# Kernel optimization log

Measured on AMD Instinct MI355X. Metric: run time of the kernel, lower is better.

Reference implementation:

```python
import jax, jax.numpy as jnp
import numpy as np

B, N, E, H, ID = 32, 256, 512, 8, 8
D = E // H  # head dim = 64


def setup_inputs() -> dict:
    key = jax.random.key(0)
    ks = jax.random.split(key, 6)
    s = lambda k, shape, fan_in: jax.random.normal(k, shape, jnp.float32) * (fan_in ** -0.5)
    return {
        "x": jax.random.normal(ks[0], (B, N, E), jnp.float32),
        "U": jax.random.normal(ks[1], (B, N, N, ID), jnp.float32),
        "w_qkv": s(ks[2], (3 * E, E), E),   # nn.MultiheadAttention in_proj_weight
        "b_qkv": jnp.zeros((3 * E,), jnp.float32),
        "w_out": s(ks[3], (E, E), E),       # out_proj.weight
        "b_out": jnp.zeros((E,), jnp.float32),
        "w_u": s(ks[4], (H, ID), ID),       # u_proj.weight
        "b_u": jnp.zeros((H,), jnp.float32),
    }


def reference(x, U, w_qkv, b_qkv, w_out, b_out, w_u, b_u):
    # fused QKV projection (torch MHA uses a single in_proj)
    qkv = x @ w_qkv.T + b_qkv                      # [B,N,3E]
    q, k, v = jnp.split(qkv, 3, axis=-1)
    split_heads = lambda t: t.reshape(B, N, H, D).transpose(0, 2, 1, 3)  # [B,H,N,D]
    q, k, v = split_heads(q), split_heads(k), split_heads(v)
    # interaction tensor -> one additive bias per head: [B,N,N,H] -> [B,H,N,N]
    bias = (U @ w_u.T + b_u).transpose(0, 3, 1, 2)
    logits = jnp.einsum('bhnd,bhmd->bhnm', q, k) * (D ** -0.5) + bias  # [B,H,N,N]
    attn = jax.nn.softmax(logits, axis=-1)
    o = jnp.einsum('bhnm,bhmd->bhnd', attn, v)     # [B,H,N,D]
    o = o.transpose(0, 2, 1, 3).reshape(B, N, E)
    return o @ w_out.T + b_out
```

## Files before the change

kernel.cpp:

```cpp
#include <hip/hip_runtime.h>
#include <stdint.h>

#define Bn 32
#define Nn 256
#define En 512
#define Hn 8
#define Dn 64

typedef __attribute__((ext_vector_type(8))) short bf16x8;
typedef __attribute__((ext_vector_type(4))) short bf16x4;
typedef __attribute__((ext_vector_type(4))) float f32x4;
typedef __attribute__((ext_vector_type(4))) _Float16 h4f;

__device__ __forceinline__ unsigned short f2bf(float f){
  union{float f; uint32_t i;} v; v.f = f;
  uint32_t i = v.i;
  return (unsigned short)((i + 0x7fffu + ((i>>16)&1u)) >> 16);
}

__device__ __forceinline__ void stage16(const unsigned short* g,
                                        unsigned short* lds_wave_base,
                                        unsigned short* lds_lane){
#if __has_builtin(__builtin_amdgcn_global_load_lds)
  __builtin_amdgcn_global_load_lds(
      (const __attribute__((address_space(1))) unsigned int*)g,
      (__attribute__((address_space(3))) unsigned int*)lds_wave_base, 16, 0, 0);
  (void)lds_lane;
#else
  *(bf16x8*)lds_lane = *(const bf16x8*)g;
  (void)lds_wave_base;
#endif
}

__global__ __launch_bounds__(256) void convert_x(
    const float* __restrict__ x, unsigned short* __restrict__ xb){
  size_t i = ((size_t)blockIdx.x * 256 + threadIdx.x) * 8;
  float4 a = *(const float4*)(x + i);
  float4 b = *(const float4*)(x + i + 4);
  bf16x8 p;
  p[0]=(short)f2bf(a.x); p[1]=(short)f2bf(a.y); p[2]=(short)f2bf(a.z); p[3]=(short)f2bf(a.w);
  p[4]=(short)f2bf(b.x); p[5]=(short)f2bf(b.y); p[6]=(short)f2bf(b.z); p[7]=(short)f2bf(b.w);
  *(bf16x8*)(xb + i) = p;
}

__global__ __launch_bounds__(256) void prep_kernel(
    const float* __restrict__ x, unsigned short* __restrict__ xb,
    const float* __restrict__ U, const float* __restrict__ w_u,
    const float* __restrict__ b_u, unsigned short* __restrict__ bias16,
    const float* __restrict__ wq, unsigned short* __restrict__ wqb,
    const float* __restrict__ wo, unsigned short* __restrict__ wob){
  __shared__ float s_wu[64];
  __shared__ float s_bu[8];
  const int bx = blockIdx.x;
  const int tid = threadIdx.x;
  if (bx < 2048 || bx >= 4096) {
    const float* src; unsigned short* dst; size_t i;
    if (bx < 2048)      { src = x;  dst = xb;  i = ((size_t)bx * 256 + tid) * 8; }
    else if (bx < 4480) { src = wq; dst = wqb; i = ((size_t)(bx-4096) * 256 + tid) * 8; }
    else                { src = wo; dst = wob; i = ((size_t)(bx-4480) * 256 + tid) * 8; }
    float4 a = *(const float4*)(src + i);
    float4 b = *(const float4*)(src + i + 4);
    bf16x8 p;
    p[0]=(short)f2bf(a.x); p[1]=(short)f2bf(a.y); p[2]=(short)f2bf(a.z); p[3]=(short)f2bf(a.w);
    p[4]=(short)f2bf(b.x); p[5]=(short)f2bf(b.y); p[6]=(short)f2bf(b.z); p[7]=(short)f2bf(b.w);
    *(bf16x8*)(dst + i) = p;
    return;
  }
  if (tid < 64) s_wu[tid] = w_u[tid];
  if (tid < 8)  s_bu[tid] = b_u[tid];
  __syncthreads();
  const int t  = (bx - 2048) * 256 + tid;
  const int m_ = t & 255;
  const int n4 = (t >> 8) & 63;
  const int bb = t >> 14;
  const float* up = U + ((size_t)(bb*Nn + n4*4)*Nn + m_) * 8;
  float u[4][8];
  #pragma unroll
  for (int r = 0; r < 4; ++r) {
    float4 a = *(const float4*)(up + (size_t)r * (Nn*8));
    float4 c = *(const float4*)(up + (size_t)r * (Nn*8) + 4);
    u[r][0]=a.x; u[r][1]=a.y; u[r][2]=a.z; u[r][3]=a.w;
    u[r][4]=c.x; u[r][5]=c.y; u[r][6]=c.z; u[r][7]=c.w;
  }
  const int    lane_in = ((n4 & 3) * 16 + (m_ & 15)) * 4;
  const size_t tbase   = ((size_t)(n4 >> 2) * 16 + (m_ >> 4)) * 256;
  #pragma unroll
  for (int h = 0; h < 8; ++h) {
    const float bu = s_bu[h];
    float acc[4];
    #pragma unroll
    for (int r = 0; r < 4; ++r) {
      float a = bu;
      #pragma unroll
      for (int id = 0; id < 8; ++id) a += u[r][id] * s_wu[h*8 + id];
      acc[r] = a;
    }
    h4f hv;
    hv[0]=(_Float16)acc[0]; hv[1]=(_Float16)acc[1];
    hv[2]=(_Float16)acc[2]; hv[3]=(_Float16)acc[3];
    *(h4f*)(bias16 + (size_t)(bb*Hn + h) * 65536 + tbase + lane_in) = hv;
  }
}

__global__ __launch_bounds__(256) void qkv_gemm4(
    const unsigned short* __restrict__ xb, const unsigned short* __restrict__ wqb,
    const float* __restrict__ bq,
    unsigned short* __restrict__ q_ws, unsigned short* __restrict__ k_ws,
    unsigned short* __restrict__ v_ws){
  __shared__ unsigned short smem[32768];
  const int tid = threadIdx.x;
  const int bx = blockIdx.x;
  const int by = blockIdx.y;
  const int row0 = by * 128, n0 = bx * 128;
  const int lane = tid & 63, wv = tid >> 6;
  const int wr = wv >> 1, wc = wv & 1;
  const int lm = lane & 15, quad = lane >> 4;
  f32x4 acc[4][4] = {};

  auto stage_tile = [&](int buf, int kc){
    const int k0 = kc * 64;
    unsigned short* sa = smem + buf * 8192;
    unsigned short* sb = smem + 16384 + buf * 8192;
    #pragma unroll
    for (int i = 0; i < 4; ++i) {
      const int ci = i*256 + tid;
      const int r = ci >> 3, c = ci & 7;
      const int sc = (c ^ (r & 7)) * 8;
      stage16(xb  + (size_t)(row0 + r)*512 + k0 + sc,
              sa + (size_t)(i*256 + wv*64)*8, sa + (size_t)ci*8);
      stage16(wqb + (size_t)(n0  + r)*512 + k0 + sc,
              sb + (size_t)(i*256 + wv*64)*8, sb + (size_t)ci*8);
    }
  };

  stage_tile(0, 0);
  #pragma unroll 1
  for (int kc = 0; kc < 8; ++kc) {
    const int cur = kc & 1;
    if (kc < 7) {
      stage_tile(cur ^ 1, kc + 1);
      asm volatile("s_waitcnt vmcnt(8)" ::: "memory");
    } else {
      asm volatile("s_waitcnt vmcnt(0)" ::: "memory");
    }
    __builtin_amdgcn_s_barrier();
    __builtin_amdgcn_sched_barrier(0);
    const unsigned short* sa = smem + cur * 8192;
    const unsigned short* sb = smem + 16384 + cur * 8192;
    #pragma unroll
    for (int ks = 0; ks < 2; ++ks) {
      bf16x8 af[4], bfr[4];
      #pragma unroll
      for (int mt = 0; mt < 4; ++mt) {
        const int r = wr*64 + mt*16 + lm;
        af[mt] = *(const bf16x8*)(sa + (size_t)r*64 + (((ks*4 + quad) ^ (r & 7)) * 8));
      }
      #pragma unroll
      for (int nt = 0; nt < 4; ++nt) {
        const int r = wc*64 + nt*16 + lm;
        bfr[nt] = *(const bf16x8*)(sb + (size_t)r*64 + (((ks*4 + quad) ^ (r & 7)) * 8));
      }
      #pragma unroll
      for (int mt = 0; mt < 4; ++mt)
        #pragma unroll
        for (int nt = 0; nt < 4; ++nt)
          acc[mt][nt] = __builtin_amdgcn_mfma_f32_16x16x32_bf16(af[mt], bfr[nt], acc[mt][nt], 0, 0, 0);
    }
    __builtin_amdgcn_sched_barrier(0);
    __builtin_amdgcn_s_barrier();
  }

  const int sec = bx >> 2;
  float bias[4];
  #pragma unroll
  for (int nt = 0; nt < 4; ++nt) bias[nt] = bq[n0 + wc*64 + nt*16 + lm];
  unsigned short* tile = smem;
  if (sec < 2) {
    const float scale = (sec == 0) ? 0.125f : 1.0f;
    #pragma unroll
    for (int nt = 0; nt < 4; ++nt) {
      const int col = wc*64 + nt*16 + lm;
      #pragma unroll
      for (int mt = 0; mt < 4; ++mt)
        #pragma unroll
        for (int r = 0; r < 4; ++r) {
          const int row = wr*64 + mt*16 + quad*4 + r;
          tile[row*136 + col] = f2bf((acc[mt][nt][r] + bias[nt]) * scale);
        }
    }
  } else {
    #pragma unroll
    for (int nt = 0; nt < 4; ++nt) {
      const int col = wc*64 + nt*16 + lm;
      #pragma unroll
      for (int mt = 0; mt < 4; ++mt)
        #pragma unroll
        for (int r = 0; r < 4; ++r) {
          const int row = wr*64 + mt*16 + quad*4 + r;
          tile[col*136 + row] = f2bf(acc[mt][nt][r] + bias[nt]);
        }
    }
  }
  __syncthreads();
  if (sec < 2) {
    unsigned short* dst = (sec == 0) ? q_ws : k_ws;
    #pragma unroll
    for (int it = 0; it < 16; ++it) {
      const int rown = it*8 + (tid >> 5);
      const int col  = (tid & 31) * 4;
      bf16x4 vv = *(const bf16x4*)(tile + rown*136 + col);
      const int c = n0 + col, ch = c & 511, h = ch >> 6, d = ch & 63;
      const int grow = row0 + rown, b = grow >> 8, n = grow & 255;
      *(bf16x4*)(dst + (((size_t)b*Hn + h)*Nn + n)*Dn + d) = vv;
    }
  } else {
    const int b = row0 >> 8, nbase = row0 & 255;
    #pragma unroll
    for (int it = 0; it < 16; ++it) {
      const int c  = it*8 + (tid >> 5);
      const int n4 = (tid & 31) * 4;
      bf16x4 vv = *(const bf16x4*)(tile + c*136 + n4);
      const int ch = (n0 - 1024) + c, h = ch >> 6, d = ch & 63;
      *(bf16x4*)(v_ws + (((size_t)b*Hn + h)*Dn + d)*Nn + nbase + n4) = vv;
    }
  }
}

__global__ __launch_bounds__(256) void oproj_gemm4(
    const unsigned short* __restrict__ o_ws, const unsigned short* __restrict__ wob,
    const float* __restrict__ bo, float* __restrict__ out){
  __shared__ unsigned short smem[24576];
  const int tid = threadIdx.x;
  const int bx = blockIdx.x;
  const int by = blockIdx.y;
  const int row0 = by * 128, n0 = bx * 64;
  const int lane = tid & 63, wv = tid >> 6;
  const int wr = wv >> 1, wc = wv & 1;
  const int lm = lane & 15, quad = lane >> 4;
  f32x4 acc[4][2] = {};

  auto stage_tile = [&](int buf, int kc){
    const int k0 = kc * 64;
    unsigned short* sa = smem + buf * 8192;
    unsigned short* sb = smem + 16384 + buf * 4096;
    #pragma unroll
    for (int i = 0; i < 4; ++i) {
      const int ci = i*256 + tid;
      const int r = ci >> 3, c = ci & 7;
      const int sc = (c ^ (r & 7)) * 8;
      stage16(o_ws + (size_t)(row0 + r)*512 + k0 + sc,
              sa + (size_t)(i*256 + wv*64)*8, sa + (size_t)ci*8);
    }
    #pragma unroll
    for (int i = 0; i < 2; ++i) {
      const int ci = i*256 + tid;
      const int r = ci >> 3, c = ci & 7;
      const int sc = (c ^ (r & 7)) * 8;
      stage16(wob + (size_t)(n0 + r)*512 + k0 + sc,
              sb + (size_t)(i*256 + wv*64)*8, sb + (size_t)ci*8);
    }
  };

  stage_tile(0, 0);
  #pragma unroll 1
  for (int kc = 0; kc < 8; ++kc) {
    const int cur = kc & 1;
    if (kc < 7) {
      stage_tile(cur ^ 1, kc + 1);
      asm volatile("s_waitcnt vmcnt(6)" ::: "memory");
    } else {
      asm volatile("s_waitcnt vmcnt(0)" ::: "memory");
    }
    __builtin_amdgcn_s_barrier();
    __builtin_amdgcn_sched_barrier(0);
    const unsigned short* sa = smem + cur * 8192;
    const unsigned short* sb = smem + 16384 + cur * 4096;
    #pragma unroll
    for (int ks = 0; ks < 2; ++ks) {
      bf16x8 af[4], bfr[2];
      #pragma unroll
      for (int mt = 0; mt < 4; ++mt) {
        const int r = wr*64 + mt*16 + lm;
        af[mt] = *(const bf16x8*)(sa + (size_t)r*64 + (((ks*4 + quad) ^ (r & 7)) * 8));
      }
      #pragma unroll
      for (int nt = 0; nt < 2; ++nt) {
        const int r = wc*32 + nt*16 + lm;
        bfr[nt] = *(const bf16x8*)(sb + (size_t)r*64 + (((ks*4 + quad) ^ (r & 7)) * 8));
      }
      #pragma unroll
      for (int mt = 0; mt < 4; ++mt)
        #pragma unroll
        for (int nt = 0; nt < 2; ++nt)
          acc[mt][nt] = __builtin_amdgcn_mfma_f32_16x16x32_bf16(af[mt], bfr[nt], acc[mt][nt], 0, 0, 0);
    }
    __builtin_amdgcn_sched_barrier(0);
    __builtin_amdgcn_s_barrier();
  }
  #pragma unroll
  for (int nt = 0; nt < 2; ++nt) {
    int c = n0 + wc*32 + nt*16 + lm;
    float bias = bo[c];
    #pragma unroll
    for (int mt = 0; mt < 4; ++mt)
      #pragma unroll
      for (int r = 0; r < 4; ++r) {
        int grow = row0 + wr*64 + mt*16 + quad*4 + r;
        out[(size_t)grow*512 + c] = acc[mt][nt][r] + bias;
      }
  }
}

__global__ __launch_bounds__(256) void attn_fast(
    const unsigned short* __restrict__ bias16,
    const unsigned short* __restrict__ q_ws, const unsigned short* __restrict__ k_ws,
    const unsigned short* __restrict__ v_ws, unsigned short* __restrict__ o_ws){
  __shared__ unsigned short s_p[4][16][40];
  const int tid = threadIdx.x;
  const int wv = tid >> 6, lane = tid & 63;
  const int lm = lane & 15, quad = lane >> 4;
  const int bx = blockIdx.x;
  const int g  = (bx & 7) * 8 + ((bx >> 3) >> 4);
  const int qt = (bx >> 3) & 15;
  const int b = g >> 1, hp = g & 1;
  const int h = hp * 4 + wv;
  const size_t hb = (size_t)b * Hn + h;
  const int qt0 = qt * 16;
  const unsigned short* qp = q_ws + (hb*Nn + qt0 + lm) * Dn;
  const bf16x8 qa0 = *(const bf16x8*)(qp + quad*8);
  const bf16x8 qa1 = *(const bf16x8*)(qp + 32 + quad*8);
  const unsigned short* bt = bias16 + (hb*16 + qt) * 16 * 256 + (size_t)lane*4;
  f32x4 oa[4] = {};
  float esum[4] = {0.f, 0.f, 0.f, 0.f};
  #pragma unroll 1
  for (int ck = 0; ck < 8; ++ck) {
    f32x4 la0, la1;
    __builtin_amdgcn_s_setprio(1);
    #pragma unroll
    for (int t = 0; t < 2; ++t) {
      const int key0 = ck*32 + t*16;
      const h4f hv = *(const h4f*)(bt + (ck*2 + t) * 256);
      f32x4 c0;
      #pragma unroll
      for (int r = 0; r < 4; ++r) c0[r] = (float)hv[r];
      const unsigned short* kp = k_ws + (hb*Nn + key0 + lm) * Dn;
      c0 = __builtin_amdgcn_mfma_f32_16x16x32_bf16(qa0, *(const bf16x8*)(kp + quad*8),      c0, 0, 0, 0);
      c0 = __builtin_amdgcn_mfma_f32_16x16x32_bf16(qa1, *(const bf16x8*)(kp + 32 + quad*8), c0, 0, 0, 0);
      if (t == 0) la0 = c0; else la1 = c0;
    }
    __builtin_amdgcn_s_setprio(0);
    #pragma unroll
    for (int r = 0; r < 4; ++r) {
      la0[r] = __expf(la0[r]);
      la1[r] = __expf(la1[r]);
      esum[r] += la0[r] + la1[r];
    }
    #pragma unroll
    for (int r = 0; r < 4; ++r) {
      s_p[wv][quad*4+r][lm]      = f2bf(la0[r]);
      s_p[wv][quad*4+r][16 + lm] = f2bf(la1[r]);
    }
    const bf16x8 ap = *(const bf16x8*)&s_p[wv][lm][quad*8];
    __builtin_amdgcn_s_setprio(1);
    #pragma unroll
    for (int nt = 0; nt < 4; ++nt) {
      const bf16x8 bv = *(const bf16x8*)(v_ws + (hb*Dn + nt*16 + lm)*Nn + ck*32 + quad*8);
      oa[nt] = __builtin_amdgcn_mfma_f32_16x16x32_bf16(ap, bv, oa[nt], 0, 0, 0);
    }
    __builtin_amdgcn_s_setprio(0);
  }
  #pragma unroll
  for (int r = 0; r < 4; ++r) {
    float s = esum[r];
    #pragma unroll
    for (int msk = 1; msk < 16; msk <<= 1) s += __shfl_xor(s, msk);
    const float inv = 1.0f / s;
    const int n = qt0 + quad*4 + r;
    #pragma unroll
    for (int nt = 0; nt < 4; ++nt)
      o_ws[((size_t)(b*Nn + n))*En + h*64 + nt*16 + lm] = f2bf(oa[nt][r] * inv);
  }
}

__global__ __launch_bounds__(256) void qkv_gemm(
    const unsigned short* __restrict__ xb, const float* __restrict__ wq,
    const float* __restrict__ bq,
    unsigned short* __restrict__ q_ws, unsigned short* __restrict__ k_ws,
    unsigned short* __restrict__ v_ws){
  __shared__ unsigned short s_a[128][40];
  __shared__ unsigned short s_b[128][40];
  const int tid = threadIdx.x;
  const int bx = blockIdx.x;
  const int by = blockIdx.y;
  const int row0 = by * 128, n0 = bx * 128;
  const int lane = tid & 63, wv = tid >> 6;
  const int wr = wv >> 1, wc = wv & 1;
  const int lm = lane & 15, quad = lane >> 4;
  const int sr = tid >> 3, sc4 = (tid & 7) * 4;
  f32x4 acc[4][4] = {};
  for (int kc = 0; kc < 16; ++kc) {
    const int k0 = kc * 32;
    __syncthreads();
    #pragma unroll
    for (int i = 0; i < 2; ++i) {
      int g = tid * 2 + i;
      int r = g >> 2, c8 = (g & 3) * 8;
      *(bf16x8*)&s_a[r][c8] = *(const bf16x8*)(xb + (size_t)(row0 + r)*512 + k0 + c8);
    }
    #pragma unroll
    for (int i = 0; i < 4; ++i) {
      int r = sr + i * 32;
      float4 vb = *(const float4*)(wq + (size_t)(n0 + r) * 512 + k0 + sc4);
      bf16x4 pb;
      pb[0]=(short)f2bf(vb.x); pb[1]=(short)f2bf(vb.y); pb[2]=(short)f2bf(vb.z); pb[3]=(short)f2bf(vb.w);
      *(bf16x4*)&s_b[r][sc4] = pb;
    }
    __syncthreads();
    bf16x8 af[4], bfr[4];
    #pragma unroll
    for (int mt = 0; mt < 4; ++mt) af[mt]  = *(const bf16x8*)&s_a[wr*64 + mt*16 + lm][quad*8];
    #pragma unroll
    for (int nt = 0; nt < 4; ++nt) bfr[nt] = *(const bf16x8*)&s_b[wc*64 + nt*16 + lm][quad*8];
    #pragma unroll
    for (int mt = 0; mt < 4; ++mt)
      #pragma unroll
      for (int nt = 0; nt < 4; ++nt)
        acc[mt][nt] = __builtin_amdgcn_mfma_f32_16x16x32_bf16(af[mt], bfr[nt], acc[mt][nt], 0, 0, 0);
  }
  #pragma unroll
  for (int nt = 0; nt < 4; ++nt) {
    int c = n0 + wc*64 + nt*16 + lm;
    float bias = bq[c];
    int sec = c >> 9, ch = c & 511, h = ch >> 6, d = ch & 63;
    #pragma unroll
    for (int mt = 0; mt < 4; ++mt) {
      #pragma unroll
      for (int r = 0; r < 4; ++r) {
        int grow = row0 + wr*64 + mt*16 + quad*4 + r;
        int b = grow >> 8, n = grow & 255;
        float val = acc[mt][nt][r] + bias;
        if (sec == 0)      q_ws[(((size_t)b*Hn + h)*Nn + n)*Dn + d] = f2bf(val * 0.125f);
        else if (sec == 1) k_ws[(((size_t)b*Hn + h)*Nn + n)*Dn + d] = f2bf(val);
        else               v_ws[(((size_t)b*Hn + h)*Dn + d)*Nn + n] = f2bf(val);
      }
    }
  }
}

__global__ __launch_bounds__(256) void attn_kernel(
    const float* __restrict__ U, const float* __restrict__ w_u, const float* __restrict__ b_u,
    const unsigned short* __restrict__ q_ws, const unsigned short* __restrict__ k_ws,
    const unsigned short* __restrict__ v_ws, unsigned short* __restrict__ o_ws){
  __shared__ unsigned short s_p[4][2][16][40];
  __shared__ float s_wu[64];
  __shared__ float s_bu[8];
  const int tid = threadIdx.x;
  const int wv = tid >> 6, lane = tid & 63;
  const int lm = lane & 15, quad = lane >> 4;
  const int blk = blockIdx.x;
  const int b = blk >> 4, qt0 = (blk & 15) * 16;
  if (tid < 64) s_wu[tid] = w_u[tid];
  if (tid < 8)  s_bu[tid] = b_u[tid];
  __syncthreads();
  const int h0 = wv * 2, h1 = h0 + 1;
  const size_t hb0 = (size_t)b * Hn + h0, hb1 = hb0 + 1;
  float wu0[8], wu1[8];
  #pragma unroll
  for (int i = 0; i < 8; ++i) { wu0[i] = s_wu[h0*8 + i]; wu1[i] = s_wu[h1*8 + i]; }
  const float bu0 = s_bu[h0], bu1 = s_bu[h1];
  const unsigned short* q0p = q_ws + (hb0*Nn + qt0 + lm)*Dn;
  const unsigned short* q1p = q_ws + (hb1*Nn + qt0 + lm)*Dn;
  const bf16x8 qa0 = *(const bf16x8*)(q0p + quad*8);
  const bf16x8 qa1 = *(const bf16x8*)(q0p + 32 + quad*8);
  const bf16x8 qb0 = *(const bf16x8*)(q1p + quad*8);
  const bf16x8 qb1 = *(const bf16x8*)(q1p + 32 + quad*8);
  f32x4 oa[4] = {}, ob[4] = {};
  float m0[4], m1[4], l0[4], l1[4];
  #pragma unroll
  for (int r = 0; r < 4; ++r) { m0[r] = m1[r] = -3.0e38f; l0[r] = l1[r] = 0.f; }
  const float* Ub = U + ((size_t)(b*Nn + qt0)) * Nn * 8;
  #pragma unroll 1
  for (int ck = 0; ck < 8; ++ck) {
    f32x4 la0, la1, lb0, lb1;
    #pragma unroll
    for (int t = 0; t < 2; ++t) {
      const int key0 = ck*32 + t*16;
      f32x4 c0, c1;
      #pragma unroll
      for (int r = 0; r < 4; ++r) {
        const float4* up = (const float4*)(Ub + ((size_t)(quad*4+r)*Nn + key0 + lm)*8);
        float4 ua = up[0], uc = up[1];
        c0[r] = bu0 + ua.x*wu0[0] + ua.y*wu0[1] + ua.z*wu0[2] + ua.w*wu0[3]
                    + uc.x*wu0[4] + uc.y*wu0[5] + uc.z*wu0[6] + uc.w*wu0[7];
        c1[r] = bu1 + ua.x*wu1[0] + ua.y*wu1[1] + ua.z*wu1[2] + ua.w*wu1[3]
                    + uc.x*wu1[4] + uc.y*wu1[5] + uc.z*wu1[6] + uc.w*wu1[7];
      }
      const unsigned short* k0p = k_ws + (hb0*Nn + key0 + lm)*Dn;
      const unsigned short* k1p = k_ws + (hb1*Nn + key0 + lm)*Dn;
      bf16x8 kf;
      kf = *(const bf16x8*)(k0p + quad*8);
      c0 = __builtin_amdgcn_mfma_f32_16x16x32_bf16(qa0, kf, c0, 0, 0, 0);
      kf = *(const bf16x8*)(k0p + 32 + quad*8);
      c0 = __builtin_amdgcn_mfma_f32_16x16x32_bf16(qa1, kf, c0, 0, 0, 0);
      kf = *(const bf16x8*)(k1p + quad*8);
      c1 = __builtin_amdgcn_mfma_f32_16x16x32_bf16(qb0, kf, c1, 0, 0, 0);
      kf = *(const bf16x8*)(k1p + 32 + quad*8);
      c1 = __builtin_amdgcn_mfma_f32_16x16x32_bf16(qb1, kf, c1, 0, 0, 0);
      if (t == 0) { la0 = c0; lb0 = c1; } else { la1 = c0; lb1 = c1; }
    }
    #pragma unroll
    for (int r = 0; r < 4; ++r) {
      {
        float tm = fmaxf(la0[r], la1[r]);
        #pragma unroll
        for (int msk = 1; msk < 16; msk <<= 1) tm = fmaxf(tm, __shfl_xor(tm, msk));
        float mn = fmaxf(m0[r], tm);
        float al = __expf(m0[r] - mn);
        m0[r] = mn;
        float e0 = __expf(la0[r] - mn), e1 = __expf(la1[r] - mn);
        la0[r] = e0; la1[r] = e1;
        float s = e0 + e1;
        #pragma unroll
        for (int msk = 1; msk < 16; msk <<= 1) s += __shfl_xor(s, msk);
        l0[r] = l0[r] * al + s;
        #pragma unroll
        for (int nt = 0; nt < 4; ++nt) oa[nt][r] *= al;
      }
      {
        float tm = fmaxf(lb0[r], lb1[r]);
        #pragma unroll
        for (int msk = 1; msk < 16; msk <<= 1) tm = fmaxf(tm, __shfl_xor(tm, msk));
        float mn = fmaxf(m1[r], tm);
        float al = __expf(m1[r] - mn);
        m1[r] = mn;
        float e0 = __expf(lb0[r] - mn), e1 = __expf(lb1[r] - mn);
        lb0[r] = e0; lb1[r] = e1;
        float s = e0 + e1;
        #pragma unroll
        for (int msk = 1; msk < 16; msk <<= 1) s += __shfl_xor(s, msk);
        l1[r] = l1[r] * al + s;
        #pragma unroll
        for (int nt = 0; nt < 4; ++nt) ob[nt][r] *= al;
      }
    }
    #pragma unroll
    for (int r = 0; r < 4; ++r) {
      s_p[wv][0][quad*4+r][lm]      = f2bf(la0[r]);
      s_p[wv][0][quad*4+r][16 + lm] = f2bf(la1[r]);
      s_p[wv][1][quad*4+r][lm]      = f2bf(lb0[r]);
      s_p[wv][1][quad*4+r][16 + lm] = f2bf(lb1[r]);
    }
    const bf16x8 ap0 = *(const bf16x8*)&s_p[wv][0][lm][quad*8];
    const bf16x8 ap1 = *(const bf16x8*)&s_p[wv][1][lm][quad*8];
    #pragma unroll
    for (int nt = 0; nt < 4; ++nt) {
      bf16x8 bv = *(const bf16x8*)(v_ws + (hb0*Dn + nt*16 + lm)*Nn + ck*32 + quad*8);
      oa[nt] = __builtin_amdgcn_mfma_f32_16x16x32_bf16(ap0, bv, oa[nt], 0, 0, 0);
      bv = *(const bf16x8*)(v_ws + (hb1*Dn + nt*16 + lm)*Nn + ck*32 + quad*8);
      ob[nt] = __builtin_amdgcn_mfma_f32_16x16x32_bf16(ap1, bv, ob[nt], 0, 0, 0);
    }
  }
  #pragma unroll
  for (int r = 0; r < 4; ++r) {
    const float i0 = 1.0f / l0[r], i1 = 1.0f / l1[r];
    const int n = qt0 + quad*4 + r;
    #pragma unroll
    for (int nt = 0; nt < 4; ++nt) {
      o_ws[((size_t)(b*Nn + n))*En + h0*64 + nt*16 + lm] = f2bf(oa[nt][r] * i0);
      o_ws[((size_t)(b*Nn + n))*En + h1*64 + nt*16 + lm] = f2bf(ob[nt][r] * i1);
    }
  }
}

__global__ __launch_bounds__(256) void oproj_gemm(
    const unsigned short* __restrict__ o_ws, const float* __restrict__ wo,
    const float* __restrict__ bo, float* __restrict__ out){
  __shared__ unsigned short s_a[128][40];
  __shared__ unsigned short s_b[128][40];
  const int tid = threadIdx.x;
  const int bx = blockIdx.x;
  const int by = blockIdx.y;
  const int row0 = by * 128, n0 = bx * 128;
  const int lane = tid & 63, wv = tid >> 6;
  const int wr = wv >> 1, wc = wv & 1;
  const int lm = lane & 15, quad = lane >> 4;
  const int sr = tid >> 3, sc4 = (tid & 7) * 4;
  f32x4 acc[4][4] = {};
  for (int kc = 0; kc < 16; ++kc) {
    const int k0 = kc * 32;
    __syncthreads();
    #pragma unroll
    for (int i = 0; i < 2; ++i) {
      int g = tid * 2 + i;
      int r = g >> 2, c8 = (g & 3) * 8;
      *(bf16x8*)&s_a[r][c8] = *(const bf16x8*)(o_ws + (size_t)(row0 + r)*512 + k0 + c8);
    }
    #pragma unroll
    for (int i = 0; i < 4; ++i) {
      int r = sr + i * 32;
      float4 vb = *(const float4*)(wo + (size_t)(n0 + r) * 512 + k0 + sc4);
      bf16x4 pb;
      pb[0]=(short)f2bf(vb.x); pb[1]=(short)f2bf(vb.y); pb[2]=(short)f2bf(vb.z); pb[3]=(short)f2bf(vb.w);
      *(bf16x4*)&s_b[r][sc4] = pb;
    }
    __syncthreads();
    bf16x8 af[4], bfr[4];
    #pragma unroll
    for (int mt = 0; mt < 4; ++mt) af[mt]  = *(const bf16x8*)&s_a[wr*64 + mt*16 + lm][quad*8];
    #pragma unroll
    for (int nt = 0; nt < 4; ++nt) bfr[nt] = *(const bf16x8*)&s_b[wc*64 + nt*16 + lm][quad*8];
    #pragma unroll
    for (int mt = 0; mt < 4; ++mt)
      #pragma unroll
      for (int nt = 0; nt < 4; ++nt)
        acc[mt][nt] = __builtin_amdgcn_mfma_f32_16x16x32_bf16(af[mt], bfr[nt], acc[mt][nt], 0, 0, 0);
  }
  #pragma unroll
  for (int nt = 0; nt < 4; ++nt) {
    int c = n0 + wc*64 + nt*16 + lm;
    float bias = bo[c];
    #pragma unroll
    for (int mt = 0; mt < 4; ++mt)
      #pragma unroll
      for (int r = 0; r < 4; ++r) {
        int grow = row0 + wr*64 + mt*16 + quad*4 + r;
        out[(size_t)grow*512 + c] = acc[mt][nt][r] + bias;
      }
  }
}

extern "C" void kernel_launch(void* const* d_in, const int* in_sizes, int n_in,
                              void* d_out, int out_size, void* d_ws, size_t ws_size,
                              hipStream_t stream) {
  const float* x     = (const float*)d_in[0];
  const float* U     = (const float*)d_in[1];
  const float* w_qkv = (const float*)d_in[2];
  const float* b_qkv = (const float*)d_in[3];
  const float* w_out = (const float*)d_in[4];
  const float* b_out = (const float*)d_in[5];
  const float* w_u   = (const float*)d_in[6];
  const float* b_u   = (const float*)d_in[7];
  float* out = (float*)d_out;

  const size_t per = (size_t)Bn * Hn * Nn * Dn;
  unsigned short* q_ws = (unsigned short*)d_ws;
  unsigned short* k_ws = q_ws + per;
  unsigned short* v_ws = k_ws + per;
  unsigned short* o_ws = v_ws + per;
  unsigned short* bias16 = o_ws + per;
  unsigned short* wqb = bias16 + (size_t)Bn*Hn*Nn*Nn;
  unsigned short* wob = wqb + (size_t)3*En*En;

  const size_t need = (per*4 + (size_t)Bn*Hn*Nn*Nn + (size_t)3*En*En + (size_t)En*En) * 2;

  if (ws_size >= need) {
    prep_kernel<<<dim3(4608),  dim3(256), 0, stream>>>(x, o_ws, U, w_u, b_u, bias16,
                                                       w_qkv, wqb, w_out, wob);
    qkv_gemm4 <<<dim3(12, 64), dim3(256), 0, stream>>>(o_ws, wqb, b_qkv, q_ws, k_ws, v_ws);
    attn_fast <<<dim3(1024),   dim3(256), 0, stream>>>(bias16, q_ws, k_ws, v_ws, o_ws);
    oproj_gemm4<<<dim3(8, 64), dim3(256), 0, stream>>>(o_ws, wob, b_out, out);
  } else {
    convert_x <<<dim3(2048),  dim3(256), 0, stream>>>(x, o_ws);
    qkv_gemm  <<<dim3(12, 64), dim3(256), 0, stream>>>(o_ws, w_qkv, b_qkv, q_ws, k_ws, v_ws);
    attn_kernel<<<dim3(Bn * 16), dim3(256), 0, stream>>>(U, w_u, b_u, q_ws, k_ws, v_ws, o_ws);
    oproj_gemm<<<dim3(4, 64), dim3(256), 0, stream>>>(o_ws, w_out, b_out, out);
  }
}
```

Baseline: 193.5 us.

## Co-schedule U-bias projection with QKV GEMM; double-buffer attention P tile

Moves the U→bias projection out of the prep kernel and into extra blocks of the QKV GEMM launch. The memory-bound bias work (reading the large U tensor) can then run alongside the compute-bound GEMM tiles, and the prep kernel is left doing only the bf16 conversions. In attention, the per-wave P staging buffer is double-buffered by chunk parity and the key loop is unrolled by two, so consecutive iterations can overlap without an LDS hazard. The risk is that the GEMM blocks now compete with bias blocks for CUs and bandwidth, and the GEMM uses a flattened 1D grid index.

```diff
diff --git a/kernel.cpp b/kernel.cpp
--- a/kernel.cpp
+++ b/kernel.cpp
@@ -43,74 +43,77 @@
   *(bf16x8*)(xb + i) = p;
 }
 
-__global__ __launch_bounds__(256) void prep_kernel(
+__global__ __launch_bounds__(256) void convert_all(
     const float* __restrict__ x, unsigned short* __restrict__ xb,
-    const float* __restrict__ U, const float* __restrict__ w_u,
-    const float* __restrict__ b_u, unsigned short* __restrict__ bias16,
     const float* __restrict__ wq, unsigned short* __restrict__ wqb,
     const float* __restrict__ wo, unsigned short* __restrict__ wob){
-  __shared__ float s_wu[64];
-  __shared__ float s_bu[8];
   const int bx = blockIdx.x;
   const int tid = threadIdx.x;
-  if (bx < 2048 || bx >= 4096) {
-    const float* src; unsigned short* dst; size_t i;
-    if (bx < 2048)      { src = x;  dst = xb;  i = ((size_t)bx * 256 + tid) * 8; }
-    else if (bx < 4480) { src = wq; dst = wqb; i = ((size_t)(bx-4096) * 256 + tid) * 8; }
-    else                { src = wo; dst = wob; i = ((size_t)(bx-4480) * 256 + tid) * 8; }
-    float4 a = *(const float4*)(src + i);
-    float4 b = *(const float4*)(src + i + 4);
-    bf16x8 p;
-    p[0]=(short)f2bf(a.x); p[1]=(short)f2bf(a.y); p[2]=(short)f2bf(a.z); p[3]=(short)f2bf(a.w);
-    p[4]=(short)f2bf(b.x); p[5]=(short)f2bf(b.y); p[6]=(short)f2bf(b.z); p[7]=(short)f2bf(b.w);
-    *(bf16x8*)(dst + i) = p;
-    return;
-  }
-  if (tid < 64) s_wu[tid] = w_u[tid];
-  if (tid < 8)  s_bu[tid] = b_u[tid];
-  __syncthreads();
-  const int t  = (bx - 2048) * 256 + tid;
-  const int m_ = t & 255;
-  const int n4 = (t >> 8) & 63;
-  const int bb = t >> 14;
-  const float* up = U + ((size_t)(bb*Nn + n4*4)*Nn + m_) * 8;
-  float u[4][8];
-  #pragma unroll
-  for (int r = 0; r < 4; ++r) {
-    float4 a = *(const float4*)(up + (size_t)r * (Nn*8));
-    float4 c = *(const float4*)(up + (size_t)r * (Nn*8) + 4);
-    u[r][0]=a.x; u[r][1]=a.y; u[r][2]=a.z; u[r][3]=a.w;
-    u[r][4]=c.x; u[r][5]=c.y; u[r][6]=c.z; u[r][7]=c.w;
-  }
-  const int    lane_in = ((n4 & 3) * 16 + (m_ & 15)) * 4;
-  const size_t tbase   = ((size_t)(n4 >> 2) * 16 + (m_ >> 4)) * 256;
-  #pragma unroll
-  for (int h = 0; h < 8; ++h) {
-    const float bu = s_bu[h];
-    float acc[4];
-    #pragma unroll
-    for (int r = 0; r < 4; ++r) {
-      float a = bu;
-      #pragma unroll
-      for (int id = 0; id < 8; ++id) a += u[r][id] * s_wu[h*8 + id];
-      acc[r] = a;
-    }
-    h4f hv;
-    hv[0]=(_Float16)acc[0]; hv[1]=(_Float16)acc[1];
-    hv[2]=(_Float16)acc[2]; hv[3]=(_Float16)acc[3];
-    *(h4f*)(bias16 + (size_t)(bb*Hn + h) * 65536 + tbase + lane_in) = hv;
-  }
-}
-
-__global__ __launch_bounds__(256) void qkv_gemm4(
+  const float* src; unsigned short* dst; size_t i;
+  if (bx < 2048)      { src = x;  dst = xb;  i = ((size_t)bx * 256 + tid) * 8; }
+  else if (bx < 2432) { src = wq; dst = wqb; i = ((size_t)(bx-2048) * 256 + tid) * 8; }
+  else                { src = wo; dst = wob; i = ((size_t)(bx-2432) * 256 + tid) * 8; }
+  float4 a = *(const float4*)(src + i);
+  float4 b = *(const float4*)(src + i + 4);
+  bf16x8 p;
+  p[0]=(short)f2bf(a.x); p[1]=(short)f2bf(a.y); p[2]=(short)f2bf(a.z); p[3]=(short)f2bf(a.w);
+  p[4]=(short)f2bf(b.x); p[5]=(short)f2bf(b.y); p[6]=(short)f2bf(b.z); p[7]=(short)f2bf(b.w);
+  *(bf16x8*)(dst + i) = p;
+}
+
+__global__ __launch_bounds__(256) void qkv_bias_gemm(
     const unsigned short* __restrict__ xb, const unsigned short* __restrict__ wqb,
     const float* __restrict__ bq,
+    const float* __restrict__ U, const float* __restrict__ w_u,
+    const float* __restrict__ b_u,
     unsigned short* __restrict__ q_ws, unsigned short* __restrict__ k_ws,
-    unsigned short* __restrict__ v_ws){
+    unsigned short* __restrict__ v_ws, unsigned short* __restrict__ bias16){
   __shared__ unsigned short smem[32768];
   const int tid = threadIdx.x;
-  const int bx = blockIdx.x;
-  const int by = blockIdx.y;
+  const int blk = blockIdx.x;
+
+  if (blk >= 768) {
+    float* s_wu = (float*)smem;
+    float* s_bu = (float*)(smem + 128);
+    if (tid < 64) s_wu[tid] = w_u[tid];
+    if (tid < 8)  s_bu[tid] = b_u[tid];
+    __syncthreads();
+    const int t  = (blk - 768) * 256 + tid;
+    const int m_ = t & 255;
+    const int n4 = (t >> 8) & 63;
+    const int bb = t >> 14;
+    const float* up = U + ((size_t)(bb*Nn + n4*4)*Nn + m_) * 8;
+    float u[4][8];
+    #pragma unroll
+    for (int r = 0; r < 4; ++r) {
+      float4 a = *(const float4*)(up + (size_t)r * (Nn*8));
+      float4 c = *(const float4*)(up + (size_t)r * (Nn*8) + 4);
+      u[r][0]=a.x; u[r][1]=a.y; u[r][2]=a.z; u[r][3]=a.w;
+      u[r][4]=c.x; u[r][5]=c.y; u[r][6]=c.z; u[r][7]=c.w;
+    }
+    const int    lane_in = ((n4 & 3) * 16 + (m_ & 15)) * 4;
+    const size_t tbase   = ((size_t)(n4 >> 2) * 16 + (m_ >> 4)) * 256;
+    #pragma unroll
+    for (int h = 0; h < 8; ++h) {
+      const float bu = s_bu[h];
+      float acc[4];
+      #pragma unroll
+      for (int r = 0; r < 4; ++r) {
+        float a = bu;
+        #pragma unroll
+        for (int id = 0; id < 8; ++id) a += u[r][id] * s_wu[h*8 + id];
+        acc[r] = a;
+      }
+      h4f hv;
+      hv[0]=(_Float16)acc[0]; hv[1]=(_Float16)acc[1];
+      hv[2]=(_Float16)acc[2]; hv[3]=(_Float16)acc[3];
+      *(h4f*)(bias16 + (size_t)(bb*Hn + h) * 65536 + tbase + lane_in) = hv;
+    }
+    return;
+  }
+
+  const int bx = blk % 12;
+  const int by = blk / 12;
   const int row0 = by * 128, n0 = bx * 128;
   const int lane = tid & 63, wv = tid >> 6;
   const int wr = wv >> 1, wc = wv & 1;
@@ -315,7 +318,7 @@
     const unsigned short* __restrict__ bias16,
     const unsigned short* __restrict__ q_ws, const unsigned short* __restrict__ k_ws,
     const unsigned short* __restrict__ v_ws, unsigned short* __restrict__ o_ws){
-  __shared__ unsigned short s_p[4][16][40];
+  __shared__ unsigned short s_p[4][2][16][40];
   const int tid = threadIdx.x;
   const int wv = tid >> 6, lane = tid & 63;
   const int lm = lane & 15, quad = lane >> 4;
@@ -332,7 +335,7 @@
   const unsigned short* bt = bias16 + (hb*16 + qt) * 16 * 256 + (size_t)lane*4;
   f32x4 oa[4] = {};
   float esum[4] = {0.f, 0.f, 0.f, 0.f};
-  #pragma unroll 1
+  #pragma unroll 2
   for (int ck = 0; ck < 8; ++ck) {
     f32x4 la0, la1;
     __builtin_amdgcn_s_setprio(1);
@@ -357,10 +360,10 @@
     }
     #pragma unroll
     for (int r = 0; r < 4; ++r) {
-      s_p[wv][quad*4+r][lm]      = f2bf(la0[r]);
-      s_p[wv][quad*4+r][16 + lm] = f2bf(la1[r]);
-    }
-    const bf16x8 ap = *(const bf16x8*)&s_p[wv][lm][quad*8];
+      s_p[wv][ck & 1][quad*4+r][lm]      = f2bf(la0[r]);
+      s_p[wv][ck & 1][quad*4+r][16 + lm] = f2bf(la1[r]);
+    }
+    const bf16x8 ap = *(const bf16x8*)&s_p[wv][ck & 1][lm][quad*8];
     __builtin_amdgcn_s_setprio(1);
     #pragma unroll
     for (int nt = 0; nt < 4; ++nt) {
@@ -654,9 +657,9 @@
   const size_t need = (per*4 + (size_t)Bn*Hn*Nn*Nn + (size_t)3*En*En + (size_t)En*En) * 2;
 
   if (ws_size >= need) {
-    prep_kernel<<<dim3(4608),  dim3(256), 0, stream>>>(x, o_ws, U, w_u, b_u, bias16,
-                                                       w_qkv, wqb, w_out, wob);
-    qkv_gemm4 <<<dim3(12, 64), dim3(256), 0, stream>>>(o_ws, wqb, b_qkv, q_ws, k_ws, v_ws);
+    convert_all<<<dim3(2560),  dim3(256), 0, stream>>>(x, o_ws, w_qkv, wqb, w_out, wob);
+    qkv_bias_gemm<<<dim3(2816), dim3(256), 0, stream>>>(o_ws, wqb, b_qkv, U, w_u, b_u,
+                                                        q_ws, k_ws, v_ws, bias16);
     attn_fast <<<dim3(1024),   dim3(256), 0, stream>>>(bias16, q_ws, k_ws, v_ws, o_ws);
     oproj_gemm4<<<dim3(8, 64), dim3(256), 0, stream>>>(o_ws, wob, b_out, out);
   } else {
```

After: 191.6 us. About the same (-1.0%).
